# Kernel optimization log

Measured on AMD Instinct MI355X. Metric: run time of the kernel, lower is better.

Reference implementation:

```python
import jax, jax.numpy as jnp
import numpy as np

B, T, P = 64, 20, 36
V, E, H, D = 32000, 300, 512, 512


def setup_inputs() -> dict:
    key = jax.random.key(0)
    ks = jax.random.split(key, 12)
    s = lambda k, shape, scale=0.05: (jax.random.normal(k, shape, jnp.float32) * scale)
    inp = {
        "h0": jax.random.normal(ks[0], (B, H), jnp.float32),
        "object_proposals": jax.random.normal(ks[1], (B, P, D), jnp.float32),
        "captions": jax.random.randint(ks[2], (B, T), 0, V),
        # lengths in [2, T]; force one row to max so max(decode_lengths) == T-1 (static)
        "caption_lengths": jax.random.randint(ks[3], (B, 1), 2, T + 1).at[0, 0].set(T),
        "emb_W": s(ks[4], (V, E), 0.1),
        "W_ih": s(ks[5], (4 * H, E + D)),
        "W_hh": s(ks[6], (4 * H, H)),
        "b_ih": jnp.zeros((4 * H,), jnp.float32),
        "b_hh": jnp.zeros((4 * H,), jnp.float32),
        "wh_W": s(ks[7], (H, E)), "wh_b": jnp.zeros((H,), jnp.float32),
        "wr_W": s(ks[8], (D, E)), "wr_b": jnp.zeros((D,), jnp.float32),
        "rh_W": s(ks[9], (H, D)), "rh_b": jnp.zeros((H,), jnp.float32),
        "w_W": s(ks[10], (E,)), "w_b": jnp.zeros((), jnp.float32),
        "r_W": s(ks[11], (D,)), "r_b": jnp.zeros((), jnp.float32),
    }
    return inp


def reference(h0, object_proposals, captions, caption_lengths, emb_W,
              W_ih, W_hh, b_ih, b_hh, wh_W, wh_b, wr_W, wr_b,
              rh_W, rh_b, w_W, w_b, r_W, r_b):
    lengths = caption_lengths[:, 0]
    sort_ind = jnp.argsort(-lengths)  # descending, stable
    h0s = h0[sort_ind]
    props = object_proposals[sort_ind]           # [B,P,D]
    caps = captions[sort_ind]                    # [B,T]
    dec = lengths[sort_ind] - 1                  # decode lengths
    Tmax = captions.shape[1] - 1                 # == max(decode_lengths) by construction

    emb = emb_W[caps]                            # [B,T,E]
    # Loop-invariant projections of the full embedding matrix (done once, not per step)
    WH = emb_W @ wh_W.T + wh_b                   # [V,H]
    WRp = emb_W @ wr_W.T + wr_b                  # [V,D]
    w_lin = emb_W @ w_W + w_b                    # [V]
    sum_WH = WH.sum(0)                           # [H]
    sum_WRp = WRp.sum(0)                         # [D]
    sum_wlin = w_lin.sum()                       # scalar
    RH = props @ rh_W.T + rh_b                   # [B,P,H]
    r_lin = props @ r_W + r_b                    # [B,P]
    S = props.sum(1)                             # [B,D]  (sum over proposals)
    wr_sumP = S @ WRp.T                          # [B,V]  = sum_p wr[b,v,p]
    wr_sumV = props @ sum_WRp                    # [B,P]  = sum_v wr[b,v,p]

    xs = (jnp.swapaxes(emb[:, :Tmax], 0, 1), jnp.arange(Tmax))

    def step(carry, x):
        h, c, fb = carry
        e_t, t = x
        mask = (t < dec)[:, None].astype(h.dtype)  # [B,1] active rows
        xin = jnp.concatenate([e_t, fb], axis=1)   # [B,E+D]
        gates = xin @ W_ih.T + b_ih + h @ W_hh.T + b_hh
        i, f, g, o = jnp.split(gates, 4, axis=1)
        c_new = jax.nn.sigmoid(f) * c + jax.nn.sigmoid(i) * jnp.tanh(g)
        h_new = jax.nn.sigmoid(o) * jnp.tanh(c_new)
        w = h_new @ WH.T + w_lin                               # [B,V]
        r = jnp.einsum('bph,bh->bp', RH, h_new) + r_lin        # [B,P]
        preds = w + wr_sumP + r.sum(1, keepdims=True)          # [B,V]
        att_logits = (h_new @ sum_WH + sum_wlin)[:, None] + wr_sumV + r
        att = jax.nn.softmax(att_logits, axis=1)               # [B,P]
        fb_new = jnp.einsum('bp,bpd->bd', att, props)          # [B,D]
        h = mask * h_new + (1.0 - mask) * h
        c = mask * c_new + (1.0 - mask) * c
        fb = mask * fb_new + (1.0 - mask) * fb
        return (h, c, fb), (preds * mask, att * mask)

    init = (h0s, h0s, jnp.zeros((h0.shape[0], props.shape[2]), h0.dtype))
    _, (P_seq, A_seq) = jax.lax.scan(step, init, xs)
    predictions = jnp.swapaxes(P_seq, 0, 1)  # [B,Tmax,V]
    attention = jnp.swapaxes(A_seq, 0, 1)    # [B,Tmax,P]
    return predictions, attention, caps[:, 1:], dec, sort_ind
```

## Files before the change

kernel.cpp:

```cpp
#include <hip/hip_runtime.h>

typedef unsigned short u16;
typedef __bf16 bf16t;
typedef bf16t v8bf __attribute__((ext_vector_type(8)));
typedef float v4f __attribute__((ext_vector_type(4)));

#define Bb 64
#define Tt 20
#define Tm 19
#define Pp 36
#define Vv 32000
#define Ee 300
#define Ep 320
#define Hh 512
#define Dd 512
#define Gg 2048
#define WPAD 1032

__device__ __forceinline__ u16 f2b(float f) {
    unsigned u = __builtin_bit_cast(unsigned, f);
    unsigned r = u + 0x7fffu + ((u >> 16) & 1u);
    return (u16)(r >> 16);
}
__device__ __forceinline__ float b2f(u16 x) {
    return __builtin_bit_cast(float, (unsigned)x << 16);
}
__device__ __forceinline__ v8bf ld8(const u16* p) {
    return *reinterpret_cast<const v8bf*>(p);
}

__device__ __forceinline__ float ld_f32_coh(const float* p) {
    return __hip_atomic_load(p, __ATOMIC_RELAXED, __HIP_MEMORY_SCOPE_AGENT);
}
__device__ __forceinline__ void st_f32_coh(float* p, float v) {
    __hip_atomic_store(p, v, __ATOMIC_RELAXED, __HIP_MEMORY_SCOPE_AGENT);
}
__device__ __forceinline__ void st_u32_coh(unsigned* p, unsigned v) {
    __hip_atomic_store(p, v, __ATOMIC_RELAXED, __HIP_MEMORY_SCOPE_AGENT);
}

__global__ void k_sentinel_r4(float* __restrict__ out, float val)
{
    int i = blockIdx.x * 256 + threadIdx.x;
    if (i < 8192) out[i] = val;
}

template<int EPI>
__global__ __launch_bounds__(256) void gemm_bt_r4(
    const u16* __restrict__ A, const u16* __restrict__ B,
    int lda, int ldb, int K,
    float* __restrict__ Cf, u16* __restrict__ Cb, int ldc,
    const float* __restrict__ addN, const float* __restrict__ addM,
    const u16* __restrict__ addMatB,
    const u16* __restrict__ wspB, const int* __restrict__ dec,
    float* __restrict__ outP)
{
    int bn = blockIdx.x, bm = blockIdx.y;
    const int tid = threadIdx.x;
    const int w = tid >> 6, l = tid & 63;
    const int lr = l & 15, lk = (l >> 4) << 3;
    const int m0 = bm * 64;
    const int n0 = bn * 64 + w * 16;
    const u16* Ap = A + (size_t)(m0 + lr) * lda + lk;
    const u16* Bp = B + (size_t)(n0 + lr) * ldb + lk;
    v4f acc0 = {0.f,0.f,0.f,0.f}, acc1 = {0.f,0.f,0.f,0.f},
        acc2 = {0.f,0.f,0.f,0.f}, acc3 = {0.f,0.f,0.f,0.f};
    for (int k = 0; k < K; k += 32) {
        v8bf bf = ld8(Bp + k);
        v8bf a0 = ld8(Ap + k);
        v8bf a1 = ld8(Ap + (size_t)16 * lda + k);
        v8bf a2 = ld8(Ap + (size_t)32 * lda + k);
        v8bf a3 = ld8(Ap + (size_t)48 * lda + k);
        acc0 = __builtin_amdgcn_mfma_f32_16x16x32_bf16(a0, bf, acc0, 0, 0, 0);
        acc1 = __builtin_amdgcn_mfma_f32_16x16x32_bf16(a1, bf, acc1, 0, 0, 0);
        acc2 = __builtin_amdgcn_mfma_f32_16x16x32_bf16(a2, bf, acc2, 0, 0, 0);
        acc3 = __builtin_amdgcn_mfma_f32_16x16x32_bf16(a3, bf, acc3, 0, 0, 0);
    }
    v4f accs[4] = {acc0, acc1, acc2, acc3};
    const int crow0 = (l >> 4) * 4;
    const int n = n0 + lr;
    #pragma unroll
    for (int i = 0; i < 4; ++i) {
        #pragma unroll
        for (int r = 0; r < 4; ++r) {
            int m = m0 + i * 16 + crow0 + r;
            float v = accs[i][r];
            if (EPI == 0) {
                if (addN) v += addN[n];
                Cf[(size_t)m * ldc + n] = v;
            } else if (EPI == 1) {
                Cb[(size_t)m * ldc + n] = f2b(v);
            } else if (EPI == 4) {
                Cb[(size_t)m * ldc + n] = f2b(v + addN[n]);
            } else if (EPI == 5) {
                Cb[(size_t)m * ldc + n] = f2b(v + addM[m]);
            }
        }
    }
}

__global__ __launch_bounds__(256) void k_pred_r10(
    const u16* __restrict__ A,
    const u16* __restrict__ B,
    const float* __restrict__ addN,
    const float* __restrict__ addM,
    const u16* __restrict__ wspB,
    const int* __restrict__ dec,
    float* __restrict__ outP)
{
    const int wg = blockIdx.x;
    const int xcd = wg & 7;
    const int g = wg >> 3;
    const int bn_local = g / 19;
    const int bm = g - bn_local * 19;
    const int nt = (xcd < 5) ? 16 : 15;
    if (bn_local >= nt) return;
    const int bn = ((xcd < 5) ? xcd * 16 : 80 + (xcd - 5) * 15) + bn_local;
    const int t = bm;
    const int n0 = bn * 256;

    __shared__ u16 As[64][72];
    __shared__ u16 Bs[256][72];

    const int tid = threadIdx.x;
    const int w = tid >> 6, l = tid & 63;
    const int lr = l & 15, lk = (l >> 4) << 3;
    const int crow0 = (l >> 4) * 4;

    v4f acc[4][4];
    #pragma unroll
    for (int i = 0; i < 4; ++i)
        #pragma unroll
        for (int j = 0; j < 4; ++j) acc[i][j] = (v4f){0.f,0.f,0.f,0.f};

    const int arow = tid >> 3;
    const int ac8  = (tid & 7) << 3;

    for (int kc = 0; kc < 5; ++kc) {
        const int k0 = kc * 64;
        __syncthreads();
        #pragma unroll
        for (int s = 0; s < 2; ++s) {
            int slot = tid + s * 256;
            int row = slot >> 3, c8 = (slot & 7) << 3;
            *reinterpret_cast<v8bf*>(&As[row][c8]) =
                ld8(A + (size_t)(t * 64 + row) * Ep + k0 + c8);
        }
        #pragma unroll
        for (int s = 0; s < 8; ++s) {
            int slot = tid + s * 256;
            int row = slot >> 3, c8 = (slot & 7) << 3;
            *reinterpret_cast<v8bf*>(&Bs[row][c8]) =
                ld8(B + (size_t)(n0 + row) * Ep + k0 + c8);
        }
        __syncthreads();
        #pragma unroll
        for (int ks = 0; ks < 2; ++ks) {
            const int kk = ks * 32 + lk;
            v8bf a0 = *reinterpret_cast<const v8bf*>(&As[lr][kk]);
            v8bf a1 = *reinterpret_cast<const v8bf*>(&As[16 + lr][kk]);
            v8bf a2 = *reinterpret_cast<const v8bf*>(&As[32 + lr][kk]);
            v8bf a3 = *reinterpret_cast<const v8bf*>(&As[48 + lr][kk]);
            #pragma unroll
            for (int j = 0; j < 4; ++j) {
                v8bf bf = *reinterpret_cast<const v8bf*>(&Bs[w * 64 + j * 16 + lr][kk]);
                acc[0][j] = __builtin_amdgcn_mfma_f32_16x16x32_bf16(a0, bf, acc[0][j], 0, 0, 0);
                acc[1][j] = __builtin_amdgcn_mfma_f32_16x16x32_bf16(a1, bf, acc[1][j], 0, 0, 0);
                acc[2][j] = __builtin_amdgcn_mfma_f32_16x16x32_bf16(a2, bf, acc[2][j], 0, 0, 0);
                acc[3][j] = __builtin_amdgcn_mfma_f32_16x16x32_bf16(a3, bf, acc[3][j], 0, 0, 0);
            }
        }
    }
    (void)arow; (void)ac8;

    float aN[4];
    #pragma unroll
    for (int j = 0; j < 4; ++j) aN[j] = addN[n0 + w * 64 + j * 16 + lr];
    #pragma unroll
    for (int i = 0; i < 4; ++i) {
        #pragma unroll
        for (int r = 0; r < 4; ++r) {
            int b = i * 16 + crow0 + r;
            float aM = addM[t * 64 + b];
            bool live = t < dec[b];
            #pragma unroll
            for (int j = 0; j < 4; ++j) {
                int n = n0 + w * 64 + j * 16 + lr;
                float x = aN[j] + aM + b2f(wspB[(size_t)b * Vv + n]);
                float v = acc[i][j][r] + x;
                outP[((size_t)b * Tm + t) * Vv + n] = live ? v : 0.0f;
            }
        }
    }
}

__device__ __forceinline__ void gbar_r7(int* flags, int epoch) {
    __syncthreads();
    if (threadIdx.x == 0)
        __hip_atomic_store(&flags[blockIdx.x * 16], epoch,
                           __ATOMIC_RELAXED, __HIP_MEMORY_SCOPE_AGENT);
    if (threadIdx.x < 64) {
        while (__hip_atomic_load(&flags[threadIdx.x * 16],
                                 __ATOMIC_RELAXED, __HIP_MEMORY_SCOPE_AGENT) < epoch)
            __builtin_amdgcn_s_sleep(1);
    }
    __syncthreads();
}

__global__ __launch_bounds__(256) void k_loop_r9(
    const u16* __restrict__ Wc, const u16* __restrict__ gates_e,
    float* __restrict__ gates,
    const float* __restrict__ sum_WH, const float* __restrict__ sum_wl,
    const float* __restrict__ wr_sumV, const float* __restrict__ r_lin,
    const float* __restrict__ RH, const u16* __restrict__ props_bf,
    const int* __restrict__ dec_i, const float* __restrict__ wh_b,
    const float* __restrict__ h_state, const float* __restrict__ c_state,
    const float* __restrict__ fb_state, u16* __restrict__ xin2s,
    u16* __restrict__ Hseq, float* __restrict__ rsum,
    float* __restrict__ out_att, int* __restrict__ flags)
{
    const int blk = blockIdx.x;
    const int tid = threadIdx.x;
    const int w = tid >> 6, l = tid & 63;
    const int lr = l & 15, lk = (l >> 4) << 3;
    const int m0 = w * 16;
    const int j0 = blk * 32;
    const int crow0 = (l >> 4) * 4;

    __shared__ u16 wlds[32][WPAD];
    __shared__ u16 plds[Pp * Dd];
    __shared__ float hbuf[Hh];
    __shared__ float rbuf[Pp];
    __shared__ float attbuf[Pp];
    __shared__ float red1[256], red2[256];
    __shared__ unsigned xbuf32[512];
    u16* xb = (u16*)xbuf32;

    for (int idx = tid; idx < 32 * 128; idx += 256) {
        int row = idx >> 7, c8 = (idx & 127) << 3;
        *reinterpret_cast<v8bf*>(&wlds[row][c8]) =
            ld8(Wc + (size_t)(j0 + row) * 1024 + c8);
    }
    for (int idx = tid; idx < (Pp * Dd) / 8; idx += 256) {
        int off = idx << 3;
        *reinterpret_cast<v8bf*>(&plds[off]) =
            ld8(props_bf + (size_t)blk * (Pp * Dd) + off);
    }

    const int b = blk;
    const int dec_b = dec_i[b];
    const float swh0 = sum_WH[tid], swh1 = sum_WH[tid + 256];
    const float wb0 = wh_b[tid], wb1 = wh_b[tid + 256];
    const float sumwl = sum_wl[0];
    const float wrsV = (tid < Pp) ? wr_sumV[b * Pp + tid] : 0.f;
    float rlin[9];
    #pragma unroll
    for (int i = 0; i < 9; ++i) rlin[i] = r_lin[b * Pp + (w + i * 4)];
    float cr0 = c_state[b * Hh + tid],       cr1 = c_state[b * Hh + tid + 256];
    float hr0 = h_state[b * Hh + tid],       hr1 = h_state[b * Hh + tid + 256];
    float fbr0 = fb_state[b * Hh + tid],     fbr1 = fb_state[b * Hh + tid + 256];
    __syncthreads();

    for (int t = 0; t < Tm; ++t) {
        {
            const u16* Ap = xin2s + (size_t)t * (Bb * 1024)
                                  + (size_t)(m0 + lr) * 1024 + lk;
            v8bf areg[32];
            #pragma unroll
            for (int k = 0; k < 32; ++k) areg[k] = ld8(Ap + k * 32);
            const u16* ge = gates_e + (size_t)t * (Bb * Gg);
            u16 ge0[4], ge1[4];
            size_t obase[4];
            #pragma unroll
            for (int r = 0; r < 4; ++r) {
                int bb = m0 + crow0 + r;
                size_t o0 = (size_t)bb * Gg + j0 + lr;
                obase[r] = o0;
                ge0[r] = ge[o0];
                ge1[r] = ge[o0 + 16];
            }
            v4f acc0 = {0.f,0.f,0.f,0.f}, acc1 = {0.f,0.f,0.f,0.f};
            #pragma unroll
            for (int k = 0; k < 32; ++k) {
                v8bf b0 = *reinterpret_cast<const v8bf*>(&wlds[lr][lk + k * 32]);
                v8bf b1 = *reinterpret_cast<const v8bf*>(&wlds[lr + 16][lk + k * 32]);
                acc0 = __builtin_amdgcn_mfma_f32_16x16x32_bf16(areg[k], b0, acc0, 0, 0, 0);
                acc1 = __builtin_amdgcn_mfma_f32_16x16x32_bf16(areg[k], b1, acc1, 0, 0, 0);
            }
            #pragma unroll
            for (int r = 0; r < 4; ++r) {
                st_f32_coh(&gates[obase[r]],      acc0[r] + b2f(ge0[r]));
                st_f32_coh(&gates[obase[r] + 16], acc1[r] + b2f(ge1[r]));
            }
        }
        gbar_r7(flags, 2 * t + 1);
        {
            bool live = t < dec_b;
            float hn_arr[2];
            const float* g = gates + (size_t)b * Gg;
            float gv[8];
            #pragma unroll
            for (int q = 0; q < 2; ++q) {
                int d = tid + q * 256;
                gv[q*4+0] = ld_f32_coh(g + d);
                gv[q*4+1] = ld_f32_coh(g + 512 + d);
                gv[q*4+2] = ld_f32_coh(g + 1024 + d);
                gv[q*4+3] = ld_f32_coh(g + 1536 + d);
            }
            #pragma unroll
            for (int q = 0; q < 2; ++q) {
                int d = tid + q * 256;
                float gi = gv[q*4+0], gf = gv[q*4+1],
                      gg2 = gv[q*4+2], go = gv[q*4+3];
                float c_old = (q == 0) ? cr0 : cr1;
                float si = 1.f / (1.f + expf(-gi));
                float sf = 1.f / (1.f + expf(-gf));
                float so = 1.f / (1.f + expf(-go));
                float cn = sf * c_old + si * tanhf(gg2);
                float hn = so * tanhf(cn);
                hbuf[d] = hn;
                hn_arr[q] = hn;
                Hseq[((size_t)t * Bb + b) * Hh + d] = f2b(hn);
                if (live) {
                    if (q == 0) { cr0 = cn; hr0 = hn; }
                    else        { cr1 = cn; hr1 = hn; }
                }
                xb[Hh + d] = f2b((q == 0) ? hr0 : hr1);
            }
            red1[tid] = hn_arr[0] * swh0 + hn_arr[1] * swh1;
            red2[tid] = hn_arr[0] * wb0 + hn_arr[1] * wb1;
            __syncthreads();
            {
                float hv[8];
                #pragma unroll
                for (int j = 0; j < 8; ++j) hv[j] = hbuf[l + j * 64];
                float rhv[9][8];
                #pragma unroll
                for (int i = 0; i < 9; ++i) {
                    const float* rh = RH + ((size_t)b * Pp + (w + i * 4)) * Dd + l;
                    #pragma unroll
                    for (int j = 0; j < 8; ++j) rhv[i][j] = rh[j * 64];
                }
                #pragma unroll
                for (int i = 0; i < 9; ++i) {
                    float a = 0.f;
                    #pragma unroll
                    for (int j = 0; j < 8; ++j) a += rhv[i][j] * hv[j];
                    #pragma unroll
                    for (int off = 32; off > 0; off >>= 1) a += __shfl_down(a, off);
                    if (l == 0) rbuf[w + i * 4] = a + rlin[i];
                }
            }
            __syncthreads();
            for (int s = 128; s > 0; s >>= 1) {
                if (tid < s) { red1[tid] += red1[tid + s]; red2[tid] += red2[tid + s]; }
                __syncthreads();
            }
            if (tid < 64) {
                float hs = red1[0] + sumwl;
                float logit = -3.4e38f;
                if (tid < Pp) logit = hs + wrsV + rbuf[tid];
                float mx = logit;
                for (int off = 32; off > 0; off >>= 1) mx = fmaxf(mx, __shfl_down(mx, off));
                mx = __shfl(mx, 0);
                float ex = (tid < Pp) ? expf(logit - mx) : 0.f;
                float sm = ex;
                for (int off = 32; off > 0; off >>= 1) sm += __shfl_down(sm, off);
                sm = __shfl(sm, 0);
                float att = ex / sm;
                float rs = (tid < Pp) ? rbuf[tid] : 0.f;
                for (int off = 32; off > 0; off >>= 1) rs += __shfl_down(rs, off);
                if (tid == 0) rsum[t * Bb + b] = rs + red2[0];
                if (tid < Pp) {
                    attbuf[tid] = att;
                    out_att[((size_t)b * Tm + t) * Pp + tid] = live ? att : 0.f;
                }
            }
            __syncthreads();
            #pragma unroll
            for (int q = 0; q < 2; ++q) {
                int d = tid + q * 256;
                float fbn = 0.f;
                for (int pp = 0; pp < Pp; ++pp)
                    fbn += attbuf[pp] * b2f(plds[pp * Dd + d]);
                if (live) { if (q == 0) fbr0 = fbn; else fbr1 = fbn; }
                xb[d] = f2b((q == 0) ? fbr0 : fbr1);
            }
            __syncthreads();
            {
                unsigned* xg = (unsigned*)(xin2s + (size_t)(t + 1) * (Bb * 1024)
                                                 + (size_t)b * 1024);
                st_u32_coh(xg + tid, xbuf32[tid]);
                st_u32_coh(xg + tid + 256, xbuf32[tid + 256]);
            }
        }
        gbar_r7(flags, 2 * t + 2);
    }
}


__global__ void k_sort_r4(const int* __restrict__ lengths,
                          int* __restrict__ sort_ind, int* __restrict__ dec_i,
                          float* __restrict__ out_dec, float* __restrict__ out_sort,
                          int* __restrict__ flags)
{
    __shared__ int len[64];
    int i = threadIdx.x;
    #pragma unroll
    for (int j = 0; j < 16; ++j) flags[i * 16 + j] = 0;
    len[i] = lengths[i];
    __syncthreads();
    int li = len[i];
    int rank = 0;
    for (int j = 0; j < 64; ++j) {
        int lj = len[j];
        rank += (lj > li) || (lj == li && j < i);
    }
    sort_ind[rank] = i;
    dec_i[rank] = li - 1;
    out_sort[rank] = (float)i;
    out_dec[rank] = (float)(li - 1);
}

__global__ void k_gather_r4(const float* __restrict__ h0, const int* __restrict__ captions,
                            const int* __restrict__ sort_ind,
                            float* __restrict__ h_state, float* __restrict__ c_state,
                            float* __restrict__ fb_state, u16* __restrict__ xin2,
                            int* __restrict__ caps_s, float* __restrict__ out_caps)
{
    int b = blockIdx.x, tid = threadIdx.x;
    int src = sort_ind[b];
    for (int d = tid; d < Hh; d += 256) {
        float v = h0[(size_t)src * Hh + d];
        h_state[b * Hh + d] = v;
        c_state[b * Hh + d] = v;
        fb_state[b * Hh + d] = 0.f;
        xin2[(size_t)b * 1024 + d] = 0;
        xin2[(size_t)b * 1024 + Hh + d] = f2b(v);
    }
    if (tid < Tt) {
        int cp = captions[src * Tt + tid];
        caps_s[b * Tt + tid] = cp;
        if (tid >= 1) out_caps[b * Tm + (tid - 1)] = (float)cp;
    }
}

__global__ void k_props_r4(const float* __restrict__ props, const int* __restrict__ sort_ind,
                           const float* __restrict__ wr_b,
                           u16* __restrict__ props_bf, u16* __restrict__ S_bf,
                           float* __restrict__ swrb)
{
    int b = blockIdx.x, tid = threadIdx.x;
    int src = sort_ind[b];
    float s0 = 0.f, s1 = 0.f;
    for (int pp = 0; pp < Pp; ++pp) {
        size_t si = ((size_t)src * Pp + pp) * Dd;
        size_t di = ((size_t)b * Pp + pp) * Dd;
        float v0 = props[si + tid];
        float v1 = props[si + tid + 256];
        props_bf[di + tid] = f2b(v0);
        props_bf[di + tid + 256] = f2b(v1);
        s0 += v0; s1 += v1;
    }
    S_bf[b * Dd + tid] = f2b(s0);
    S_bf[b * Dd + tid + 256] = f2b(s1);
    float part = s0 * wr_b[tid] + s1 * wr_b[tid + 256];
    __shared__ float red[256];
    red[tid] = part;
    __syncthreads();
    for (int s = 128; s > 0; s >>= 1) {
        if (tid < s) red[tid] += red[tid + s];
        __syncthreads();
    }
    if (tid == 0) swrb[b] = red[0];
}

__global__ void k_embcast_r4(const float* __restrict__ emb_W, const float* __restrict__ w_W,
                             const float* __restrict__ w_b,
                             u16* __restrict__ embp, float* __restrict__ w_lin)
{
    int v = blockIdx.x * 4 + (threadIdx.x >> 6);
    int l = threadIdx.x & 63;
    if (v >= Vv) return;
    float acc = 0.f;
    for (int e = l; e < Ep; e += 64) {
        float x = (e < Ee) ? emb_W[(size_t)v * Ee + e] : 0.f;
        embp[(size_t)v * Ep + e] = f2b(x);
        if (e < Ee) acc += x * w_W[e];
    }
    for (int off = 32; off > 0; off >>= 1) acc += __shfl_down(acc, off);
    if (l == 0) w_lin[v] = acc + w_b[0];
}

__global__ void k_colsumA_r4(const float* __restrict__ emb_W, float* __restrict__ partial)
{
    int blk = blockIdx.x, e = threadIdx.x;
    float s = 0.f;
    int r0 = blk * 100;
    if (e < Ee)
        for (int r = 0; r < 100; ++r) s += emb_W[(size_t)(r0 + r) * Ee + e];
    partial[blk * Ep + e] = (e < Ee) ? s : 0.f;
}

__global__ void k_colsumB_r4(const float* __restrict__ partial, const float* __restrict__ w_W,
                             const float* __restrict__ w_b,
                             float* __restrict__ colsum, float* __restrict__ sum_wl)
{
    int e = threadIdx.x;
    float s = 0.f;
    for (int b = 0; b < 320; ++b) s += partial[b * Ep + e];
    colsum[e] = s;
    __shared__ float red[512];
    red[e] = (e < Ee) ? s * w_W[e] : 0.f;
    if (e < 192) red[320 + e] = 0.f;
    __syncthreads();
    for (int st = 256; st > 0; st >>= 1) {
        if (e < st) red[e] += red[e + st];
        __syncthreads();
    }
    if (e == 0) sum_wl[0] = red[0] + 32000.f * w_b[0];
}

__global__ void k_sums_r4(const float* __restrict__ colsum,
                          const float* __restrict__ wh_W, const float* __restrict__ wh_b,
                          const float* __restrict__ wr_W, const float* __restrict__ wr_b,
                          float* __restrict__ sum_WH, float* __restrict__ sum_WRp)
{
    int g = blockIdx.x * 64 + threadIdx.x;
    const float* W; const float* bias; float* out; int idx;
    if (g < Hh) { W = wh_W; bias = wh_b; out = sum_WH; idx = g; }
    else { W = wr_W; bias = wr_b; out = sum_WRp; idx = g - Hh; }
    float s = 0.f;
    for (int e = 0; e < Ee; ++e) s += colsum[e] * W[(size_t)idx * Ee + e];
    out[idx] = s + 32000.f * bias[idx];
}

__global__ void k_rlin_r4(const u16* __restrict__ props_bf, const float* __restrict__ r_W,
                          const float* __restrict__ r_b, const float* __restrict__ sum_WRp,
                          float* __restrict__ r_lin, float* __restrict__ wr_sumV)
{
    int b = blockIdx.x;
    int w = threadIdx.x >> 6, l = threadIdx.x & 63;
    for (int pp = w; pp < Pp; pp += 4) {
        const u16* row = props_bf + ((size_t)b * Pp + pp) * Dd;
        float a = 0.f, c = 0.f;
        for (int d = l; d < Dd; d += 64) {
            float x = b2f(row[d]);
            a += x * r_W[d];
            c += x * sum_WRp[d];
        }
        for (int off = 32; off > 0; off >>= 1) {
            a += __shfl_down(a, off);
            c += __shfl_down(c, off);
        }
        if (l == 0) {
            r_lin[b * Pp + pp] = a + r_b[0];
            wr_sumV[b * Pp + pp] = c;
        }
    }
}

__global__ void k_castwc_r4(const float* __restrict__ W_ih, const float* __restrict__ W_hh,
                            u16* __restrict__ Wc, u16* __restrict__ WihE)
{
    int j = blockIdx.x * 4 + (threadIdx.x >> 6);
    int l = threadIdx.x & 63;
    for (int k = l; k < 1024; k += 64) {
        float v = (k < 512) ? W_ih[(size_t)j * 812 + 300 + k]
                            : W_hh[(size_t)j * 512 + (k - 512)];
        Wc[(size_t)j * 1024 + k] = f2b(v);
    }
    for (int e = l; e < Ep; e += 64) {
        float v = (e < Ee) ? W_ih[(size_t)j * 812 + e] : 0.f;
        WihE[(size_t)j * Ep + e] = f2b(v);
    }
}

__global__ void k_castwh_r4(const float* __restrict__ wh_W, const float* __restrict__ wr_W,
                            u16* __restrict__ BtWh, u16* __restrict__ BtWr)
{
    int e = blockIdx.x;
    const float* W; u16* O;
    if (e < Ep) { W = wh_W; O = BtWh; }
    else { W = wr_W; O = BtWr; e -= Ep; }
    for (int h = threadIdx.x; h < Hh; h += 256) {
        float v = (e < Ee) ? W[(size_t)h * Ee + e] : 0.f;
        O[(size_t)e * Hh + h] = f2b(v);
    }
}

__global__ void k_castrh_r4(const float* __restrict__ rh_W, u16* __restrict__ rh_bf)
{
    int h = blockIdx.x * 4 + (threadIdx.x >> 6);
    int l = threadIdx.x & 63;
    for (int d = l; d < Dd; d += 64)
        rh_bf[(size_t)h * Dd + d] = f2b(rh_W[(size_t)h * Dd + d]);
}

__global__ void k_biascat_r4(const float* __restrict__ b_ih, const float* __restrict__ b_hh,
                             float* __restrict__ bias_cat)
{
    int j = blockIdx.x * 256 + threadIdx.x;
    bias_cat[j] = b_ih[j] + b_hh[j];
}

__global__ void k_embs_r4(const u16* __restrict__ embp, const int* __restrict__ caps_s,
                          u16* __restrict__ emb_s)
{
    int m = blockIdx.x * 4 + (threadIdx.x >> 6);
    int l = threadIdx.x & 63;
    int t = m >> 6, b = m & 63;
    int cap = caps_s[b * Tt + t];
    cap = cap < 0 ? 0 : (cap > Vv - 1 ? Vv - 1 : cap);
    const u16* src = embp + (size_t)cap * Ep;
    u16* dst = emb_s + (size_t)m * Ep;
    for (int e = l; e < Ep; e += 64) dst[e] = src[e];
}

extern "C" void kernel_launch(void* const* d_in, const int* in_sizes, int n_in,
                              void* d_out, int out_size, void* d_ws, size_t ws_size,
                              hipStream_t stream) {
    float* out = (float*)d_out;
    float* out_pred = out;
    float* out_att  = out + (size_t)Bb * Tm * Vv;
    float* out_caps = out_att + (size_t)Bb * Tm * Pp;
    float* out_dec  = out_caps + Bb * Tm;
    float* out_sort = out_dec + Bb;

    if (n_in != 19) {
        k_sentinel_r4<<<32, 256, 0, stream>>>(out_pred, 10240.f);
        return;
    }
    static const int exp_sizes[19] = {
        Bb * Hh, Bb * Pp * Dd, Bb * Tt, Bb, Vv * Ee,
        Gg * (Ee + Dd), Gg * Hh, Gg, Gg,
        Hh * Ee, Hh, Dd * Ee, Dd, Hh * Dd, Hh, Ee, 1, Dd, 1
    };
    for (int i = 0; i < 19; ++i) {
        if (in_sizes[i] != exp_sizes[i]) {
            k_sentinel_r4<<<32, 256, 0, stream>>>(out_pred, 10752.f + 256.f * i);
            return;
        }
    }
    const int exp_out = Bb * Tm * Vv + Bb * Tm * Pp + Bb * Tm + Bb + Bb;
    if (out_size != exp_out) {
        k_sentinel_r4<<<32, 256, 0, stream>>>(out_pred, 11264.f);
        return;
    }

    char* p = (char*)d_ws;
    auto alloc = [&](size_t bytes) -> char* {
        char* r = p;
        p += (bytes + 255) & ~(size_t)255;
        return r;
    };
    int*   i_sort   = (int*)alloc(Bb * 4);
    int*   i_dec    = (int*)alloc(Bb * 4);
    int*   caps_s   = (int*)alloc(Bb * Tt * 4);
    float* h_state  = (float*)alloc(Bb * Hh * 4);
    float* c_state  = (float*)alloc(Bb * Hh * 4);
    float* fb_state = (float*)alloc(Bb * Hh * 4);
    float* swrb     = (float*)alloc(Bb * 4);
    float* gates    = (float*)alloc((size_t)Bb * Gg * 4);
    float* rsum     = (float*)alloc(Tm * Bb * 4);
    float* colsum   = (float*)alloc(Ep * 4);
    float* partialc = (float*)alloc(320 * Ep * 4);
    float* w_lin    = (float*)alloc((size_t)Vv * 4);
    float* sum_WH   = (float*)alloc(Hh * 4);
    float* sum_WRp  = (float*)alloc(Dd * 4);
    float* sum_wl   = (float*)alloc(256);
    float* r_lin    = (float*)alloc(Bb * Pp * 4);
    float* wr_sumV  = (float*)alloc(Bb * Pp * 4);
    float* bias_cat = (float*)alloc(Gg * 4);
    float* RH       = (float*)alloc((size_t)Bb * Pp * Hh * 4);
    int*   flags    = (int*)alloc(Bb * 16 * 4);
    u16*   gates_e  = (u16*)alloc((size_t)Tm * Bb * Gg * 2);
    u16*   wr_sumP  = (u16*)alloc((size_t)Bb * Vv * 2);
    u16*   embp     = (u16*)alloc((size_t)Vv * Ep * 2);
    u16*   emb_s    = (u16*)alloc((size_t)Tm * Bb * Ep * 2);
    u16*   BtWh     = (u16*)alloc((size_t)Ep * Hh * 2);
    u16*   BtWr     = (u16*)alloc((size_t)Ep * Hh * 2);
    u16*   rh_bf    = (u16*)alloc((size_t)Hh * Dd * 2);
    u16*   WihE     = (u16*)alloc((size_t)Gg * Ep * 2);
    u16*   Wc       = (u16*)alloc((size_t)Gg * 1024 * 2);
    u16*   props_bf = (u16*)alloc((size_t)Bb * Pp * Dd * 2);
    u16*   S_bf     = (u16*)alloc(Bb * Dd * 2);
    u16*   Sw       = (u16*)alloc(Bb * Ep * 2);
    u16*   xin2s    = (u16*)alloc((size_t)(Tm + 1) * Bb * 1024 * 2);
    u16*   Hseq     = (u16*)alloc((size_t)Tm * Bb * Hh * 2);
    u16*   Hw       = (u16*)alloc((size_t)Tm * Bb * Ep * 2);
    size_t needed = (size_t)(p - (char*)d_ws);
    if (ws_size < needed) {
        k_sentinel_r4<<<32, 256, 0, stream>>>(out_pred, 10496.f);
        return;
    }

    const float* h0      = (const float*)d_in[0];
    const float* props   = (const float*)d_in[1];
    const int*   captions= (const int*)d_in[2];
    const int*   cap_len = (const int*)d_in[3];
    const float* emb_W   = (const float*)d_in[4];
    const float* W_ih    = (const float*)d_in[5];
    const float* W_hh    = (const float*)d_in[6];
    const float* b_ih    = (const float*)d_in[7];
    const float* b_hh    = (const float*)d_in[8];
    const float* wh_W    = (const float*)d_in[9];
    const float* wh_b    = (const float*)d_in[10];
    const float* wr_W    = (const float*)d_in[11];
    const float* wr_b    = (const float*)d_in[12];
    const float* rh_W    = (const float*)d_in[13];
    const float* rh_b    = (const float*)d_in[14];
    const float* w_W     = (const float*)d_in[15];
    const float* w_b     = (const float*)d_in[16];
    const float* r_W     = (const float*)d_in[17];
    const float* r_b     = (const float*)d_in[18];

    k_sort_r4<<<1, 64, 0, stream>>>(cap_len, i_sort, i_dec, out_dec, out_sort, flags);
    k_biascat_r4<<<Gg / 256, 256, 0, stream>>>(b_ih, b_hh, bias_cat);
    k_embcast_r4<<<Vv / 4, 256, 0, stream>>>(emb_W, w_W, w_b, embp, w_lin);
    k_colsumA_r4<<<320, 320, 0, stream>>>(emb_W, partialc);
    k_colsumB_r4<<<1, 320, 0, stream>>>(partialc, w_W, w_b, colsum, sum_wl);
    k_sums_r4<<<16, 64, 0, stream>>>(colsum, wh_W, wh_b, wr_W, wr_b, sum_WH, sum_WRp);
    k_gather_r4<<<Bb, 256, 0, stream>>>(h0, captions, i_sort, h_state, c_state,
                                        fb_state, xin2s, caps_s, out_caps);
    k_props_r4<<<Bb, 256, 0, stream>>>(props, i_sort, wr_b, props_bf, S_bf, swrb);
    k_rlin_r4<<<Bb, 256, 0, stream>>>(props_bf, r_W, r_b, sum_WRp, r_lin, wr_sumV);
    k_castwc_r4<<<Gg / 4, 256, 0, stream>>>(W_ih, W_hh, Wc, WihE);
    k_castwh_r4<<<2 * Ep, 256, 0, stream>>>(wh_W, wr_W, BtWh, BtWr);
    k_castrh_r4<<<Hh / 4, 256, 0, stream>>>(rh_W, rh_bf);
    k_embs_r4<<<(Tm * Bb) / 4, 256, 0, stream>>>(embp, caps_s, emb_s);

    gemm_bt_r4<4><<<dim3(Gg / 64, (Tm * Bb) / 64), 256, 0, stream>>>(
        emb_s, WihE, Ep, Ep, Ep, nullptr, gates_e, Gg,
        bias_cat, nullptr, nullptr, nullptr, nullptr, nullptr);
    gemm_bt_r4<0><<<dim3(Hh / 64, (Bb * Pp) / 64), 256, 0, stream>>>(
        props_bf, rh_bf, Dd, Dd, Dd, RH, nullptr, Hh,
        rh_b, nullptr, nullptr, nullptr, nullptr, nullptr);
    gemm_bt_r4<1><<<dim3(Ep / 64, 1), 256, 0, stream>>>(
        S_bf, BtWr, Dd, Hh, Dd, nullptr, Sw, Ep,
        nullptr, nullptr, nullptr, nullptr, nullptr, nullptr);
    gemm_bt_r4<5><<<dim3(Vv / 64, 1), 256, 0, stream>>>(
        Sw, embp, Ep, Ep, Ep, nullptr, wr_sumP, Vv,
        nullptr, swrb, nullptr, nullptr, nullptr, nullptr);

    k_loop_r9<<<Bb, 256, 0, stream>>>(Wc, gates_e, gates, sum_WH, sum_wl, wr_sumV,
                                      r_lin, RH, props_bf, i_dec, wh_b,
                                      h_state, c_state, fb_state, xin2s, Hseq,
                                      rsum, out_att, flags);

    gemm_bt_r4<1><<<dim3(Ep / 64, (Tm * Bb) / 64), 256, 0, stream>>>(
        Hseq, BtWh, Hh, Hh, Hh, nullptr, Hw, Ep,
        nullptr, nullptr, nullptr, nullptr, nullptr, nullptr);
    k_pred_r10<<<dim3(8 * 304), 256, 0, stream>>>(
        Hw, embp, w_lin, rsum, wr_sumP, i_dec, out_pred);
}
```

Before: 662.8 us.

## Prefetch next K chunk in registers and store B tiles in MFMA fragment order

```diff
diff --git a/kernel.cpp b/kernel.cpp
--- a/kernel.cpp
+++ b/kernel.cpp
@@ -15,7 +15,6 @@
 #define Hh 512
 #define Dd 512
 #define Gg 2048
-#define WPAD 1032
 
 __device__ __forceinline__ u16 f2b(float f) {
     unsigned u = __builtin_bit_cast(unsigned, f);
@@ -99,7 +98,7 @@
     }
 }
 
-__global__ __launch_bounds__(256) void k_pred_r10(
+__global__ __launch_bounds__(256) void k_pred_r11(
     const u16* __restrict__ A,
     const u16* __restrict__ B,
     const float* __restrict__ addN,
@@ -119,8 +118,8 @@
     const int t = bm;
     const int n0 = bn * 256;
 
-    __shared__ u16 As[64][72];
-    __shared__ u16 Bs[256][72];
+    __shared__ u16 BT[2][4][4][64][8];
+    u16* BTf = (u16*)BT;
 
     const int tid = threadIdx.x;
     const int w = tid >> 6, l = tid & 63;
@@ -133,45 +132,70 @@
         #pragma unroll
         for (int j = 0; j < 4; ++j) acc[i][j] = (v4f){0.f,0.f,0.f,0.f};
 
-    const int arow = tid >> 3;
-    const int ac8  = (tid & 7) << 3;
-
+    int brow[8], bcol[8];
+    #pragma unroll
+    for (int s = 0; s < 8; ++s) {
+        int slot = tid + s * 256;
+        int ks = slot >> 10, wq = (slot >> 8) & 3, j = (slot >> 6) & 3, ln = slot & 63;
+        brow[s] = n0 + wq * 64 + j * 16 + (ln & 15);
+        bcol[s] = ks * 32 + ((ln >> 4) << 3);
+    }
+
+    v8bf bstg[8];
+    #pragma unroll
+    for (int s = 0; s < 8; ++s)
+        bstg[s] = ld8(B + (size_t)brow[s] * Ep + 0 + bcol[s]);
+    v8bf areg[2][4];
+    #pragma unroll
+    for (int ks = 0; ks < 2; ++ks)
+        #pragma unroll
+        for (int i = 0; i < 4; ++i)
+            areg[ks][i] = ld8(A + (size_t)(t * 64 + i * 16 + lr) * Ep + 0 + ks * 32 + lk);
+    #pragma unroll
+    for (int s = 0; s < 8; ++s)
+        *reinterpret_cast<v8bf*>(&BTf[(size_t)(tid + s * 256) * 8]) = bstg[s];
+    __syncthreads();
+
+    #pragma unroll
     for (int kc = 0; kc < 5; ++kc) {
-        const int k0 = kc * 64;
-        __syncthreads();
-        #pragma unroll
-        for (int s = 0; s < 2; ++s) {
-            int slot = tid + s * 256;
-            int row = slot >> 3, c8 = (slot & 7) << 3;
-            *reinterpret_cast<v8bf*>(&As[row][c8]) =
-                ld8(A + (size_t)(t * 64 + row) * Ep + k0 + c8);
-        }
-        #pragma unroll
-        for (int s = 0; s < 8; ++s) {
-            int slot = tid + s * 256;
-            int row = slot >> 3, c8 = (slot & 7) << 3;
-            *reinterpret_cast<v8bf*>(&Bs[row][c8]) =
-                ld8(B + (size_t)(n0 + row) * Ep + k0 + c8);
-        }
-        __syncthreads();
+        v8bf bnxt[8];
+        v8bf anxt[2][4];
+        if (kc < 4) {
+            const int k0n = (kc + 1) * 64;
+            #pragma unroll
+            for (int s = 0; s < 8; ++s)
+                bnxt[s] = ld8(B + (size_t)brow[s] * Ep + k0n + bcol[s]);
+            #pragma unroll
+            for (int ks = 0; ks < 2; ++ks)
+                #pragma unroll
+                for (int i = 0; i < 4; ++i)
+                    anxt[ks][i] = ld8(A + (size_t)(t * 64 + i * 16 + lr) * Ep
+                                        + k0n + ks * 32 + lk);
+        }
         #pragma unroll
         for (int ks = 0; ks < 2; ++ks) {
-            const int kk = ks * 32 + lk;
-            v8bf a0 = *reinterpret_cast<const v8bf*>(&As[lr][kk]);
-            v8bf a1 = *reinterpret_cast<const v8bf*>(&As[16 + lr][kk]);
-            v8bf a2 = *reinterpret_cast<const v8bf*>(&As[32 + lr][kk]);
-            v8bf a3 = *reinterpret_cast<const v8bf*>(&As[48 + lr][kk]);
             #pragma unroll
             for (int j = 0; j < 4; ++j) {
-                v8bf bf = *reinterpret_cast<const v8bf*>(&Bs[w * 64 + j * 16 + lr][kk]);
-                acc[0][j] = __builtin_amdgcn_mfma_f32_16x16x32_bf16(a0, bf, acc[0][j], 0, 0, 0);
-                acc[1][j] = __builtin_amdgcn_mfma_f32_16x16x32_bf16(a1, bf, acc[1][j], 0, 0, 0);
-                acc[2][j] = __builtin_amdgcn_mfma_f32_16x16x32_bf16(a2, bf, acc[2][j], 0, 0, 0);
-                acc[3][j] = __builtin_amdgcn_mfma_f32_16x16x32_bf16(a3, bf, acc[3][j], 0, 0, 0);
-            }
-        }
-    }
-    (void)arow; (void)ac8;
+                v8bf bf = *reinterpret_cast<const v8bf*>(&BT[ks][w][j][l][0]);
+                acc[0][j] = __builtin_amdgcn_mfma_f32_16x16x32_bf16(areg[ks][0], bf, acc[0][j], 0, 0, 0);
+                acc[1][j] = __builtin_amdgcn_mfma_f32_16x16x32_bf16(areg[ks][1], bf, acc[1][j], 0, 0, 0);
+                acc[2][j] = __builtin_amdgcn_mfma_f32_16x16x32_bf16(areg[ks][2], bf, acc[2][j], 0, 0, 0);
+                acc[3][j] = __builtin_amdgcn_mfma_f32_16x16x32_bf16(areg[ks][3], bf, acc[3][j], 0, 0, 0);
+            }
+        }
+        if (kc < 4) {
+            __syncthreads();
+            #pragma unroll
+            for (int s = 0; s < 8; ++s)
+                *reinterpret_cast<v8bf*>(&BTf[(size_t)(tid + s * 256) * 8]) = bnxt[s];
+            #pragma unroll
+            for (int ks = 0; ks < 2; ++ks)
+                #pragma unroll
+                for (int i = 0; i < 4; ++i)
+                    areg[ks][i] = anxt[ks][i];
+            __syncthreads();
+        }
+    }
 
     float aN[4];
     #pragma unroll
@@ -207,7 +231,7 @@
     __syncthreads();
 }
 
-__global__ __launch_bounds__(256) void k_loop_r9(
+__global__ __launch_bounds__(256) void k_loop_r11(
     const u16* __restrict__ Wc, const u16* __restrict__ gates_e,
     float* __restrict__ gates,
     const float* __restrict__ sum_WH, const float* __restrict__ sum_wl,
@@ -227,7 +251,7 @@
     const int j0 = blk * 32;
     const int crow0 = (l >> 4) * 4;
 
-    __shared__ u16 wlds[32][WPAD];
+    __shared__ u16 wldsT[32][2][64][8];
     __shared__ u16 plds[Pp * Dd];
     __shared__ float hbuf[Hh];
     __shared__ float rbuf[Pp];
@@ -235,11 +259,15 @@
     __shared__ float red1[256], red2[256];
     __shared__ unsigned xbuf32[512];
     u16* xb = (u16*)xbuf32;
-
-    for (int idx = tid; idx < 32 * 128; idx += 256) {
-        int row = idx >> 7, c8 = (idx & 127) << 3;
-        *reinterpret_cast<v8bf*>(&wlds[row][c8]) =
-            ld8(Wc + (size_t)(j0 + row) * 1024 + c8);
+    u16* wldsf = (u16*)wldsT;
+
+    #pragma unroll
+    for (int s = 0; s < 16; ++s) {
+        int slot = tid + s * 256;
+        int k = slot >> 7, h = (slot >> 6) & 1, ln = slot & 63;
+        *reinterpret_cast<v8bf*>(&wldsf[(size_t)slot * 8]) =
+            ld8(Wc + (size_t)(j0 + h * 16 + (ln & 15)) * 1024
+                   + k * 32 + ((ln >> 4) << 3));
     }
     for (int idx = tid; idx < (Pp * Dd) / 8; idx += 256) {
         int off = idx << 3;
@@ -282,8 +310,8 @@
             v4f acc0 = {0.f,0.f,0.f,0.f}, acc1 = {0.f,0.f,0.f,0.f};
             #pragma unroll
             for (int k = 0; k < 32; ++k) {
-                v8bf b0 = *reinterpret_cast<const v8bf*>(&wlds[lr][lk + k * 32]);
-                v8bf b1 = *reinterpret_cast<const v8bf*>(&wlds[lr + 16][lk + k * 32]);
+                v8bf b0 = *reinterpret_cast<const v8bf*>(&wldsT[k][0][l][0]);
+                v8bf b1 = *reinterpret_cast<const v8bf*>(&wldsT[k][1][l][0]);
                 acc0 = __builtin_amdgcn_mfma_f32_16x16x32_bf16(areg[k], b0, acc0, 0, 0, 0);
                 acc1 = __builtin_amdgcn_mfma_f32_16x16x32_bf16(areg[k], b1, acc1, 0, 0, 0);
             }
@@ -743,14 +771,14 @@
         Sw, embp, Ep, Ep, Ep, nullptr, wr_sumP, Vv,
         nullptr, swrb, nullptr, nullptr, nullptr, nullptr);
 
-    k_loop_r9<<<Bb, 256, 0, stream>>>(Wc, gates_e, gates, sum_WH, sum_wl, wr_sumV,
-                                      r_lin, RH, props_bf, i_dec, wh_b,
-                                      h_state, c_state, fb_state, xin2s, Hseq,
-                                      rsum, out_att, flags);
+    k_loop_r11<<<Bb, 256, 0, stream>>>(Wc, gates_e, gates, sum_WH, sum_wl, wr_sumV,
+                                       r_lin, RH, props_bf, i_dec, wh_b,
+                                       h_state, c_state, fb_state, xin2s, Hseq,
+                                       rsum, out_att, flags);
 
     gemm_bt_r4<1><<<dim3(Ep / 64, (Tm * Bb) / 64), 256, 0, stream>>>(
         Hseq, BtWh, Hh, Hh, Hh, nullptr, Hw, Ep,
         nullptr, nullptr, nullptr, nullptr, nullptr, nullptr);
-    k_pred_r10<<<dim3(8 * 304), 256, 0, stream>>>(
+    k_pred_r11<<<dim3(8 * 304), 256, 0, stream>>>(
         Hw, embp, w_lin, rsum, wr_sumP, i_dec, out_pred);
 }
```

After: 724.1 us. +9.2%, slower.

## Fuse prep casts into one launch, pre-swizzle LSTM weights in LDS, hoist RH loads

Applied to the files above, without the earlier changes.

```diff
diff --git a/kernel.cpp b/kernel.cpp
--- a/kernel.cpp
+++ b/kernel.cpp
@@ -15,7 +15,6 @@
 #define Hh 512
 #define Dd 512
 #define Gg 2048
-#define WPAD 1032
 
 __device__ __forceinline__ u16 f2b(float f) {
     unsigned u = __builtin_bit_cast(unsigned, f);
@@ -133,9 +132,6 @@
         #pragma unroll
         for (int j = 0; j < 4; ++j) acc[i][j] = (v4f){0.f,0.f,0.f,0.f};
 
-    const int arow = tid >> 3;
-    const int ac8  = (tid & 7) << 3;
-
     for (int kc = 0; kc < 5; ++kc) {
         const int k0 = kc * 64;
         __syncthreads();
@@ -171,7 +167,6 @@
             }
         }
     }
-    (void)arow; (void)ac8;
 
     float aN[4];
     #pragma unroll
@@ -207,7 +202,7 @@
     __syncthreads();
 }
 
-__global__ __launch_bounds__(256) void k_loop_r9(
+__global__ __launch_bounds__(256) void k_loop_r12(
     const u16* __restrict__ Wc, const u16* __restrict__ gates_e,
     float* __restrict__ gates,
     const float* __restrict__ sum_WH, const float* __restrict__ sum_wl,
@@ -227,7 +222,7 @@
     const int j0 = blk * 32;
     const int crow0 = (l >> 4) * 4;
 
-    __shared__ u16 wlds[32][WPAD];
+    __shared__ u16 wldsT[32][2][64][8];
     __shared__ u16 plds[Pp * Dd];
     __shared__ float hbuf[Hh];
     __shared__ float rbuf[Pp];
@@ -235,11 +230,15 @@
     __shared__ float red1[256], red2[256];
     __shared__ unsigned xbuf32[512];
     u16* xb = (u16*)xbuf32;
-
-    for (int idx = tid; idx < 32 * 128; idx += 256) {
-        int row = idx >> 7, c8 = (idx & 127) << 3;
-        *reinterpret_cast<v8bf*>(&wlds[row][c8]) =
-            ld8(Wc + (size_t)(j0 + row) * 1024 + c8);
+    u16* wldsf = (u16*)wldsT;
+
+    #pragma unroll
+    for (int s = 0; s < 16; ++s) {
+        int slot = tid + s * 256;
+        int k = slot >> 7, h = (slot >> 6) & 1, ln = slot & 63;
+        *reinterpret_cast<v8bf*>(&wldsf[(size_t)slot * 8]) =
+            ld8(Wc + (size_t)(j0 + h * 16 + (ln & 15)) * 1024
+                   + k * 32 + ((ln >> 4) << 3));
     }
     for (int idx = tid; idx < (Pp * Dd) / 8; idx += 256) {
         int off = idx << 3;
@@ -256,6 +255,13 @@
     float rlin[9];
     #pragma unroll
     for (int i = 0; i < 9; ++i) rlin[i] = r_lin[b * Pp + (w + i * 4)];
+    float rhv[9][8];
+    #pragma unroll
+    for (int i = 0; i < 9; ++i) {
+        const float* rh = RH + ((size_t)b * Pp + (w + i * 4)) * Dd + l;
+        #pragma unroll
+        for (int j = 0; j < 8; ++j) rhv[i][j] = rh[j * 64];
+    }
     float cr0 = c_state[b * Hh + tid],       cr1 = c_state[b * Hh + tid + 256];
     float hr0 = h_state[b * Hh + tid],       hr1 = h_state[b * Hh + tid + 256];
     float fbr0 = fb_state[b * Hh + tid],     fbr1 = fb_state[b * Hh + tid + 256];
@@ -282,8 +288,8 @@
             v4f acc0 = {0.f,0.f,0.f,0.f}, acc1 = {0.f,0.f,0.f,0.f};
             #pragma unroll
             for (int k = 0; k < 32; ++k) {
-                v8bf b0 = *reinterpret_cast<const v8bf*>(&wlds[lr][lk + k * 32]);
-                v8bf b1 = *reinterpret_cast<const v8bf*>(&wlds[lr + 16][lk + k * 32]);
+                v8bf b0 = *reinterpret_cast<const v8bf*>(&wldsT[k][0][l][0]);
+                v8bf b1 = *reinterpret_cast<const v8bf*>(&wldsT[k][1][l][0]);
                 acc0 = __builtin_amdgcn_mfma_f32_16x16x32_bf16(areg[k], b0, acc0, 0, 0, 0);
                 acc1 = __builtin_amdgcn_mfma_f32_16x16x32_bf16(areg[k], b1, acc1, 0, 0, 0);
             }
@@ -334,13 +340,6 @@
                 float hv[8];
                 #pragma unroll
                 for (int j = 0; j < 8; ++j) hv[j] = hbuf[l + j * 64];
-                float rhv[9][8];
-                #pragma unroll
-                for (int i = 0; i < 9; ++i) {
-                    const float* rh = RH + ((size_t)b * Pp + (w + i * 4)) * Dd + l;
-                    #pragma unroll
-                    for (int j = 0; j < 8; ++j) rhv[i][j] = rh[j * 64];
-                }
                 #pragma unroll
                 for (int i = 0; i < 9; ++i) {
                     float a = 0.f;
@@ -398,29 +397,85 @@
     }
 }
 
-
-__global__ void k_sort_r4(const int* __restrict__ lengths,
-                          int* __restrict__ sort_ind, int* __restrict__ dec_i,
-                          float* __restrict__ out_dec, float* __restrict__ out_sort,
-                          int* __restrict__ flags)
-{
-    __shared__ int len[64];
-    int i = threadIdx.x;
-    #pragma unroll
-    for (int j = 0; j < 16; ++j) flags[i * 16 + j] = 0;
-    len[i] = lengths[i];
-    __syncthreads();
-    int li = len[i];
-    int rank = 0;
-    for (int j = 0; j < 64; ++j) {
-        int lj = len[j];
-        rank += (lj > li) || (lj == li && j < i);
-    }
-    sort_ind[rank] = i;
-    dec_i[rank] = li - 1;
-    out_sort[rank] = (float)i;
-    out_dec[rank] = (float)(li - 1);
-}
+__global__ __launch_bounds__(256) void k_prep1_r12(
+    const int* __restrict__ lengths, int* __restrict__ sort_ind,
+    int* __restrict__ dec_i, float* __restrict__ out_dec,
+    float* __restrict__ out_sort, int* __restrict__ flags,
+    const float* __restrict__ b_ih, const float* __restrict__ b_hh,
+    float* __restrict__ bias_cat,
+    const float* __restrict__ emb_W, const float* __restrict__ w_W,
+    const float* __restrict__ w_b, u16* __restrict__ embp,
+    float* __restrict__ w_lin,
+    const float* __restrict__ W_ih, const float* __restrict__ W_hh,
+    u16* __restrict__ Wc, u16* __restrict__ WihE,
+    const float* __restrict__ wh_W, const float* __restrict__ wr_W,
+    u16* __restrict__ BtWh, u16* __restrict__ BtWr,
+    const float* __restrict__ rh_W, u16* __restrict__ rh_bf)
+{
+    const int blk = blockIdx.x, tid = threadIdx.x;
+    if (blk == 0) {
+        __shared__ int len[64];
+        if (tid < 64) {
+            #pragma unroll
+            for (int j = 0; j < 16; ++j) flags[tid * 16 + j] = 0;
+            len[tid] = lengths[tid];
+        }
+        __syncthreads();
+        if (tid < 64) {
+            int li = len[tid];
+            int rank = 0;
+            for (int j = 0; j < 64; ++j) {
+                int lj = len[j];
+                rank += (lj > li) || (lj == li && j < tid);
+            }
+            sort_ind[rank] = tid;
+            dec_i[rank] = li - 1;
+            out_sort[rank] = (float)tid;
+            out_dec[rank] = (float)(li - 1);
+        }
+    } else if (blk < 9) {
+        int j = (blk - 1) * 256 + tid;
+        bias_cat[j] = b_ih[j] + b_hh[j];
+    } else if (blk < 8009) {
+        int v = (blk - 9) * 4 + (tid >> 6);
+        int l = tid & 63;
+        float acc = 0.f;
+        for (int e = l; e < Ep; e += 64) {
+            float x = (e < Ee) ? emb_W[(size_t)v * Ee + e] : 0.f;
+            embp[(size_t)v * Ep + e] = f2b(x);
+            if (e < Ee) acc += x * w_W[e];
+        }
+        for (int off = 32; off > 0; off >>= 1) acc += __shfl_down(acc, off);
+        if (l == 0) w_lin[v] = acc + w_b[0];
+    } else if (blk < 8521) {
+        int j = (blk - 8009) * 4 + (tid >> 6);
+        int l = tid & 63;
+        for (int k = l; k < 1024; k += 64) {
+            float v = (k < 512) ? W_ih[(size_t)j * 812 + 300 + k]
+                                : W_hh[(size_t)j * 512 + (k - 512)];
+            Wc[(size_t)j * 1024 + k] = f2b(v);
+        }
+        for (int e = l; e < Ep; e += 64) {
+            float v = (e < Ee) ? W_ih[(size_t)j * 812 + e] : 0.f;
+            WihE[(size_t)j * Ep + e] = f2b(v);
+        }
+    } else if (blk < 9161) {
+        int e = blk - 8521;
+        const float* W; u16* O;
+        if (e < Ep) { W = wh_W; O = BtWh; }
+        else { W = wr_W; O = BtWr; e -= Ep; }
+        for (int h = tid; h < Hh; h += 256) {
+            float v = (e < Ee) ? W[(size_t)h * Ee + e] : 0.f;
+            O[(size_t)e * Hh + h] = f2b(v);
+        }
+    } else {
+        int h = (blk - 9161) * 4 + (tid >> 6);
+        int l = tid & 63;
+        for (int d = l; d < Dd; d += 64)
+            rh_bf[(size_t)h * Dd + d] = f2b(rh_W[(size_t)h * Dd + d]);
+    }
+}
+
 
 __global__ void k_gather_r4(const float* __restrict__ h0, const int* __restrict__ captions,
                             const int* __restrict__ sort_ind,
@@ -475,23 +530,6 @@
     if (tid == 0) swrb[b] = red[0];
 }
 
-__global__ void k_embcast_r4(const float* __restrict__ emb_W, const float* __restrict__ w_W,
-                             const float* __restrict__ w_b,
-                             u16* __restrict__ embp, float* __restrict__ w_lin)
-{
-    int v = blockIdx.x * 4 + (threadIdx.x >> 6);
-    int l = threadIdx.x & 63;
-    if (v >= Vv) return;
-    float acc = 0.f;
-    for (int e = l; e < Ep; e += 64) {
-        float x = (e < Ee) ? emb_W[(size_t)v * Ee + e] : 0.f;
-        embp[(size_t)v * Ep + e] = f2b(x);
-        if (e < Ee) acc += x * w_W[e];
-    }
-    for (int off = 32; off > 0; off >>= 1) acc += __shfl_down(acc, off);
-    if (l == 0) w_lin[v] = acc + w_b[0];
-}
-
 __global__ void k_colsumA_r4(const float* __restrict__ emb_W, float* __restrict__ partial)
 {
     int blk = blockIdx.x, e = threadIdx.x;
@@ -558,50 +596,6 @@
             wr_sumV[b * Pp + pp] = c;
         }
     }
-}
-
-__global__ void k_castwc_r4(const float* __restrict__ W_ih, const float* __restrict__ W_hh,
-                            u16* __restrict__ Wc, u16* __restrict__ WihE)
-{
-    int j = blockIdx.x * 4 + (threadIdx.x >> 6);
-    int l = threadIdx.x & 63;
-    for (int k = l; k < 1024; k += 64) {
-        float v = (k < 512) ? W_ih[(size_t)j * 812 + 300 + k]
-                            : W_hh[(size_t)j * 512 + (k - 512)];
-        Wc[(size_t)j * 1024 + k] = f2b(v);
-    }
-    for (int e = l; e < Ep; e += 64) {
-        float v = (e < Ee) ? W_ih[(size_t)j * 812 + e] : 0.f;
-        WihE[(size_t)j * Ep + e] = f2b(v);
-    }
-}
-
-__global__ void k_castwh_r4(const float* __restrict__ wh_W, const float* __restrict__ wr_W,
-                            u16* __restrict__ BtWh, u16* __restrict__ BtWr)
-{
-    int e = blockIdx.x;
-    const float* W; u16* O;
-    if (e < Ep) { W = wh_W; O = BtWh; }
-    else { W = wr_W; O = BtWr; e -= Ep; }
-    for (int h = threadIdx.x; h < Hh; h += 256) {
-        float v = (e < Ee) ? W[(size_t)h * Ee + e] : 0.f;
-        O[(size_t)e * Hh + h] = f2b(v);
-    }
-}
-
-__global__ void k_castrh_r4(const float* __restrict__ rh_W, u16* __restrict__ rh_bf)
-{
-    int h = blockIdx.x * 4 + (threadIdx.x >> 6);
-    int l = threadIdx.x & 63;
-    for (int d = l; d < Dd; d += 64)
-        rh_bf[(size_t)h * Dd + d] = f2b(rh_W[(size_t)h * Dd + d]);
-}
-
-__global__ void k_biascat_r4(const float* __restrict__ b_ih, const float* __restrict__ b_hh,
-                             float* __restrict__ bias_cat)
-{
-    int j = blockIdx.x * 256 + threadIdx.x;
-    bias_cat[j] = b_ih[j] + b_hh[j];
 }
 
 __global__ void k_embs_r4(const u16* __restrict__ embp, const int* __restrict__ caps_s,
@@ -715,9 +709,13 @@
     const float* r_W     = (const float*)d_in[17];
     const float* r_b     = (const float*)d_in[18];
 
-    k_sort_r4<<<1, 64, 0, stream>>>(cap_len, i_sort, i_dec, out_dec, out_sort, flags);
-    k_biascat_r4<<<Gg / 256, 256, 0, stream>>>(b_ih, b_hh, bias_cat);
-    k_embcast_r4<<<Vv / 4, 256, 0, stream>>>(emb_W, w_W, w_b, embp, w_lin);
+    k_prep1_r12<<<9289, 256, 0, stream>>>(
+        cap_len, i_sort, i_dec, out_dec, out_sort, flags,
+        b_ih, b_hh, bias_cat,
+        emb_W, w_W, w_b, embp, w_lin,
+        W_ih, W_hh, Wc, WihE,
+        wh_W, wr_W, BtWh, BtWr,
+        rh_W, rh_bf);
     k_colsumA_r4<<<320, 320, 0, stream>>>(emb_W, partialc);
     k_colsumB_r4<<<1, 320, 0, stream>>>(partialc, w_W, w_b, colsum, sum_wl);
     k_sums_r4<<<16, 64, 0, stream>>>(colsum, wh_W, wh_b, wr_W, wr_b, sum_WH, sum_WRp);
@@ -725,9 +723,6 @@
                                         fb_state, xin2s, caps_s, out_caps);
     k_props_r4<<<Bb, 256, 0, stream>>>(props, i_sort, wr_b, props_bf, S_bf, swrb);
     k_rlin_r4<<<Bb, 256, 0, stream>>>(props_bf, r_W, r_b, sum_WRp, r_lin, wr_sumV);
-    k_castwc_r4<<<Gg / 4, 256, 0, stream>>>(W_ih, W_hh, Wc, WihE);
-    k_castwh_r4<<<2 * Ep, 256, 0, stream>>>(wh_W, wr_W, BtWh, BtWr);
-    k_castrh_r4<<<Hh / 4, 256, 0, stream>>>(rh_W, rh_bf);
     k_embs_r4<<<(Tm * Bb) / 4, 256, 0, stream>>>(embp, caps_s, emb_s);
 
     gemm_bt_r4<4><<<dim3(Gg / 64, (Tm * Bb) / 64), 256, 0, stream>>>(
@@ -743,10 +738,10 @@
         Sw, embp, Ep, Ep, Ep, nullptr, wr_sumP, Vv,
         nullptr, swrb, nullptr, nullptr, nullptr, nullptr);
 
-    k_loop_r9<<<Bb, 256, 0, stream>>>(Wc, gates_e, gates, sum_WH, sum_wl, wr_sumV,
-                                      r_lin, RH, props_bf, i_dec, wh_b,
-                                      h_state, c_state, fb_state, xin2s, Hseq,
-                                      rsum, out_att, flags);
+    k_loop_r12<<<Bb, 256, 0, stream>>>(Wc, gates_e, gates, sum_WH, sum_wl, wr_sumV,
+                                       r_lin, RH, props_bf, i_dec, wh_b,
+                                       h_state, c_state, fb_state, xin2s, Hseq,
+                                       rsum, out_att, flags);
 
     gemm_bt_r4<1><<<dim3(Ep / 64, (Tm * Bb) / 64), 256, 0, stream>>>(
         Hseq, BtWh, Hh, Hh, Hh, nullptr, Hw, Ep,
```

Result: faster. 641.4 us (-3.2%).
